# Performance work log

Hardware: AMD Instinct MI355X
Metric: run time of the kernel (lower is better)

Reference implementation:

```python
import jax, jax.numpy as jnp
import numpy as np

TEMPERATURE = 0.05
SCALE = 0.02  # keeps distances/T small enough that exp(-d/T) does not underflow


def setup_inputs() -> dict:
    key = jax.random.key(0)
    k1, k2 = jax.random.split(key)
    B, D = 4096, 1024
    text_embeddings = jax.random.normal(k1, (B, D), dtype=jnp.float32) * SCALE
    image_embeddings = jax.random.normal(k2, (B, D), dtype=jnp.float32) * SCALE
    return {"text_embeddings": text_embeddings, "image_embeddings": image_embeddings}


def reference(text_embeddings, image_embeddings):
    B = text_embeddings.shape[0]
    # Pairwise L2 distances between every image_i and every text_j without
    # materializing a [B, B, D] diff tensor: ||a||^2 + ||b||^2 - 2 a.b
    img_sq = jnp.sum(image_embeddings * image_embeddings, axis=1)   # [B]
    txt_sq = jnp.sum(text_embeddings * text_embeddings, axis=1)     # [B]
    cross = jnp.einsum('id,jd->ij', image_embeddings, text_embeddings)  # [B, B]
    sq_dist = img_sq[:, None] + txt_sq[None, :] - 2.0 * cross
    dist = jnp.sqrt(jnp.maximum(sq_dist, 0.0))                      # [B, B]
    sim = jnp.exp(-dist / TEMPERATURE)                              # [B, B]
    numerator = jnp.diagonal(sim)                                   # sim[i, i]
    denominator = jnp.sum(sim, axis=1) - numerator                  # off-diagonal row sum
    per_sample = jnp.where(denominator != 0.0,
                           -jnp.log(numerator / denominator),
                           0.0)
    return jnp.sum(per_sample) / B
```

## Files before the change

kernel.cpp:

```cpp
#include <hip/hip_runtime.h>
#include <hip/hip_bf16.h>
#include <math.h>

#define BSZ 4096
#define DSZ 1024
#define BM  256
#define BN  256
#define BK  64
#define NT  (DSZ / BK)

typedef unsigned short u16;
typedef __attribute__((ext_vector_type(8))) short bf16x8;
typedef __attribute__((ext_vector_type(4))) float f32x4;

__device__ inline u16 f2bf_rne(float f) {
    unsigned int u = __float_as_uint(f);
    u += 0x7fffu + ((u >> 16) & 1u);
    return (u16)(u >> 16);
}

__global__ __launch_bounds__(256) void cvt_norm_kernel(
        const float* __restrict__ img, const float* __restrict__ txt,
        u16* __restrict__ imgb, u16* __restrict__ txtb,
        float* __restrict__ img_sq, float* __restrict__ txt_sq,
        float* __restrict__ rowsum) {
    const int row = blockIdx.x;
    const bool isTxt = (blockIdx.y != 0);
    const float* __restrict__ src = isTxt ? txt : img;
    u16* __restrict__ dst = isTxt ? txtb : imgb;
    float* __restrict__ sq = isTxt ? txt_sq : img_sq;

    const int t = threadIdx.x;
    const float4 v = reinterpret_cast<const float4*>(src + (size_t)row * DSZ)[t];

    ushort4 o;
    o.x = f2bf_rne(v.x); o.y = f2bf_rne(v.y);
    o.z = f2bf_rne(v.z); o.w = f2bf_rne(v.w);
    reinterpret_cast<ushort4*>(dst + (size_t)row * DSZ)[t] = o;

    float s = v.x * v.x + v.y * v.y + v.z * v.z + v.w * v.w;
    #pragma unroll
    for (int off = 32; off; off >>= 1) s += __shfl_down(s, off);

    __shared__ float lds[4];
    if ((t & 63) == 0) lds[t >> 6] = s;
    __syncthreads();
    if (t == 0) {
        sq[row] = lds[0] + lds[1] + lds[2] + lds[3];
        if (!isTxt) rowsum[row] = 0.0f;
    }
}

__global__ __launch_bounds__(512, 2) void fused_mfma_kernel(
        const u16* __restrict__ imgb, const u16* __restrict__ txtb,
        const float* __restrict__ img_sq, const float* __restrict__ txt_sq,
        float* __restrict__ rowsum, float* __restrict__ diag_dist) {

    extern __shared__ char smem[];

    const int bi = blockIdx.y;
    const int bj = blockIdx.x;
    const int tid  = threadIdx.x;
    const int lane = tid & 63;
    const int w    = tid >> 6;
    const int wr   = w >> 2;
    const int wc   = w & 3;
    const int lr   = lane >> 4;
    const int lc   = lane & 15;
    const int swz  = lc & 7;

    const int ib0 = bi * BM;
    const int jb0 = bj * BN;

    const int srow = tid >> 3;
    const int sch  = tid & 7;

    f32x4 acc[8][4] = {};

    auto stage8k = [&](const u16* __restrict__ src, int xoff, int b, int h,
                       int j, int rowbase, int kt) {
        const int row_h = j * 64 + srow;
        const int gch   = sch ^ (row_h & 7);
        const u16* g = src + (size_t)(rowbase + h * 128 + row_h) * DSZ
                           + kt * BK + gch * 8;
        char* dst = smem + xoff + b * 32768 + h * 16384 + j * 8192 + w * 1024;
        __builtin_amdgcn_global_load_lds(
            (const __attribute__((address_space(1))) void*)g,
            (__attribute__((address_space(3))) void*)dst, 16, 0, 0);
    };
    auto stageA = [&](int b, int kt) {
        stage8k(imgb, 0, b, 0, 0, ib0, kt);
        stage8k(imgb, 0, b, 0, 1, ib0, kt);
        stage8k(imgb, 0, b, 1, 0, ib0, kt);
        stage8k(imgb, 0, b, 1, 1, ib0, kt);
    };
    auto stageB = [&](int b, int kt) {
        stage8k(txtb, 65536, b, 0, 0, jb0, kt);
        stage8k(txtb, 65536, b, 0, 1, jb0, kt);
        stage8k(txtb, 65536, b, 1, 0, jb0, kt);
        stage8k(txtb, 65536, b, 1, 1, jb0, kt);
    };

    const char* Abase = smem + wr * 16384;
    const char* Bbase = smem + 65536 + (wc >> 1) * 16384;
    const int rboff = (wc & 1) * 64;

    stageA(0, 0);
    stageB(0, 0);
    __syncthreads();

    int cur = 0;
    for (int kt = 0; kt < NT; ++kt) {
        const int nxt = cur ^ 1;
        bf16x8 bfr[2][4];

        #pragma unroll
        for (int p = 0; p < 4; ++p) {
            bf16x8 afr[2][2];
            if (p == 0) {
                #pragma unroll
                for (int kk = 0; kk < 2; ++kk)
                    #pragma unroll
                    for (int n = 0; n < 4; ++n) {
                        const int rb = rboff + n * 16 + lc;
                        bfr[kk][n] = *reinterpret_cast<const bf16x8*>(
                            Bbase + cur * 32768 + rb * 128
                                  + (((kk * 4 + lr) ^ swz) * 16));
                    }
            }
            #pragma unroll
            for (int dm = 0; dm < 2; ++dm)
                #pragma unroll
                for (int kk = 0; kk < 2; ++kk) {
                    const int ra = (p * 2 + dm) * 16 + lc;
                    afr[dm][kk] = *reinterpret_cast<const bf16x8*>(
                        Abase + cur * 32768 + ra * 128
                              + (((kk * 4 + lr) ^ swz) * 16));
                }

            if (kt + 1 < NT) {
                if (p == 0) stageA(nxt, kt + 1);
                else if (p == 1) stageB(nxt, kt + 1);
            }

            __builtin_amdgcn_s_barrier();
            __builtin_amdgcn_s_setprio(1);
            #pragma unroll
            for (int dm = 0; dm < 2; ++dm)
                #pragma unroll
                for (int n = 0; n < 4; ++n)
                    #pragma unroll
                    for (int kk = 0; kk < 2; ++kk)
                        acc[p * 2 + dm][n] = __builtin_amdgcn_mfma_f32_16x16x32_bf16(
                            afr[dm][kk], bfr[kk][n], acc[p * 2 + dm][n], 0, 0, 0);
            __builtin_amdgcn_s_setprio(0);
            if (p < 3) __builtin_amdgcn_s_barrier();
        }
        __syncthreads();
        cur = nxt;
    }

    const int jw = jb0 + wc * 64;
    const int iw = ib0 + wr * 128;

    float tq[4];
    #pragma unroll
    for (int n = 0; n < 4; ++n) tq[n] = txt_sq[jw + n * 16 + lc];

    float rs[8][4];
    #pragma unroll
    for (int m = 0; m < 8; ++m) {
        #pragma unroll
        for (int j = 0; j < 4; ++j) {
            const int gi = iw + m * 16 + lr * 4 + j;
            const float iq = img_sq[gi];
            float s = 0.0f;
            #pragma unroll
            for (int n = 0; n < 4; ++n) {
                const float d2 = iq + tq[n] - 2.0f * acc[m][n][j];
                const float d  = sqrtf(fmaxf(d2, 0.0f));
                const float sim = __expf(-20.0f * d);
                s += sim;
                if (gi == jw + n * 16 + lc) diag_dist[gi] = d;
            }
            rs[m][j] = s;
        }
    }

    #pragma unroll
    for (int off = 1; off < 16; off <<= 1)
        #pragma unroll
        for (int m = 0; m < 8; ++m)
            #pragma unroll
            for (int j = 0; j < 4; ++j)
                rs[m][j] += __shfl_xor(rs[m][j], off);

    if (lc == 0) {
        #pragma unroll
        for (int m = 0; m < 8; ++m)
            #pragma unroll
            for (int j = 0; j < 4; ++j)
                atomicAdd(&rowsum[iw + m * 16 + lr * 4 + j], rs[m][j]);
    }
}

__global__ __launch_bounds__(256) void finalize_kernel(
        const float* __restrict__ rowsum, const float* __restrict__ diag_dist,
        float* __restrict__ out) {
    const int tid = threadIdx.x;
    float s = 0.0f;
    for (int i = tid; i < BSZ; i += 256) {
        const float d   = diag_dist[i];
        const float num = __expf(-20.0f * d);
        const float den = rowsum[i] - num;
        s += (den != 0.0f) ? (20.0f * d + logf(den)) : 0.0f;
    }
    #pragma unroll
    for (int off = 32; off; off >>= 1) s += __shfl_down(s, off);

    __shared__ float lds[4];
    if ((tid & 63) == 0) lds[tid >> 6] = s;
    __syncthreads();
    if (tid == 0) out[0] = (lds[0] + lds[1] + lds[2] + lds[3]) * (1.0f / (float)BSZ);
}

extern "C" void kernel_launch(void* const* d_in, const int* in_sizes, int n_in,
                              void* d_out, int out_size, void* d_ws, size_t ws_size,
                              hipStream_t stream) {
    const float* txt = (const float*)d_in[0];
    const float* img = (const float*)d_in[1];
    float* out = (float*)d_out;

    u16* imgb = (u16*)d_ws;
    u16* txtb = imgb + (size_t)BSZ * DSZ;
    float* fws     = (float*)(txtb + (size_t)BSZ * DSZ);
    float* rowsum  = fws;
    float* diag    = fws + BSZ;
    float* img_sq  = fws + 2 * BSZ;
    float* txt_sq  = fws + 3 * BSZ;

    (void)hipFuncSetAttribute((const void*)fused_mfma_kernel,
                              hipFuncAttributeMaxDynamicSharedMemorySize, 131072);

    cvt_norm_kernel<<<dim3(BSZ, 2), 256, 0, stream>>>(img, txt, imgb, txtb,
                                                      img_sq, txt_sq, rowsum);

    fused_mfma_kernel<<<dim3(BSZ / BN, BSZ / BM), 512, 131072, stream>>>(
        imgb, txtb, img_sq, txt_sq, rowsum, diag);

    finalize_kernel<<<1, 256, 0, stream>>>(rowsum, diag, out);
}
```

Measured before the change: 129.0 us.

## Restructure GEMM mainloop into finer-grained staggered prefetch with explicit vmcnt waits

The k-loop now processes two k-tiles per iteration in eight phases. Each phase issues a half-tile global-to-LDS load, so the A and B prefetches for future tiles are spread across the loop and run further ahead. The full __syncthreads per tile is replaced by explicit s_waitcnt vmcnt/lgkmcnt plus s_barrier, so loads can stay in flight across phase boundaries. Block indices are also remapped to a swizzled order to improve L2 reuse between concurrently running tiles. The hand-counted vmcnt values are fragile: a wrong count could cause reads of LDS data that has not arrived yet.

```diff
diff --git a/kernel.cpp b/kernel.cpp
--- a/kernel.cpp
+++ b/kernel.cpp
@@ -7,7 +7,8 @@
 #define BM  256
 #define BN  256
 #define BK  64
-#define NT  (DSZ / BK)
+#define NT  16
+#define NIT 8
 
 typedef unsigned short u16;
 typedef __attribute__((ext_vector_type(8))) short bf16x8;
@@ -58,8 +59,10 @@
 
     extern __shared__ char smem[];
 
-    const int bi = blockIdx.y;
-    const int bj = blockIdx.x;
+    const int lin = blockIdx.y * 16 + blockIdx.x;
+    const int sw  = (lin & 7) * 32 + (lin >> 3);
+    const int bi = sw >> 4, bj = sw & 15;
+
     const int tid  = threadIdx.x;
     const int lane = tid & 63;
     const int w    = tid >> 6;
@@ -72,78 +75,77 @@
     const int ib0 = bi * BM;
     const int jb0 = bj * BN;
 
-    const int srow = tid >> 3;
-    const int sch  = tid & 7;
+    auto stageHT = [&](int mat, int kt, int h) {
+        const u16* base   = mat ? txtb : imgb;
+        const int rowbase = mat ? jb0 : ib0;
+        const int xoff    = mat ? 65536 : 0;
+        const int b = kt & 1;
+        #pragma unroll
+        for (int j = 0; j < 2; ++j) {
+            const int row_h = j * 64 + (tid >> 3);
+            const int gch   = (tid & 7) ^ (row_h & 7);
+            const u16* g = base + (size_t)(rowbase + h * 128 + row_h) * DSZ
+                                + kt * BK + gch * 8;
+            char* dst = smem + xoff + b * 32768 + h * 16384 + j * 8192 + w * 1024;
+            __builtin_amdgcn_global_load_lds(
+                (const __attribute__((address_space(1))) void*)g,
+                (__attribute__((address_space(3))) void*)dst, 16, 0, 0);
+        }
+    };
+
+    stageHT(0, 0, 0); stageHT(0, 0, 1);
+    stageHT(1, 0, 0); stageHT(1, 0, 1);
+    stageHT(1, 1, 0); stageHT(1, 1, 1);
+    asm volatile("s_waitcnt vmcnt(4)" ::: "memory");
+    __builtin_amdgcn_s_barrier();
 
     f32x4 acc[8][4] = {};
-
-    auto stage8k = [&](const u16* __restrict__ src, int xoff, int b, int h,
-                       int j, int rowbase, int kt) {
-        const int row_h = j * 64 + srow;
-        const int gch   = sch ^ (row_h & 7);
-        const u16* g = src + (size_t)(rowbase + h * 128 + row_h) * DSZ
-                           + kt * BK + gch * 8;
-        char* dst = smem + xoff + b * 32768 + h * 16384 + j * 8192 + w * 1024;
-        __builtin_amdgcn_global_load_lds(
-            (const __attribute__((address_space(1))) void*)g,
-            (__attribute__((address_space(3))) void*)dst, 16, 0, 0);
-    };
-    auto stageA = [&](int b, int kt) {
-        stage8k(imgb, 0, b, 0, 0, ib0, kt);
-        stage8k(imgb, 0, b, 0, 1, ib0, kt);
-        stage8k(imgb, 0, b, 1, 0, ib0, kt);
-        stage8k(imgb, 0, b, 1, 1, ib0, kt);
-    };
-    auto stageB = [&](int b, int kt) {
-        stage8k(txtb, 65536, b, 0, 0, jb0, kt);
-        stage8k(txtb, 65536, b, 0, 1, jb0, kt);
-        stage8k(txtb, 65536, b, 1, 0, jb0, kt);
-        stage8k(txtb, 65536, b, 1, 1, jb0, kt);
-    };
-
-    const char* Abase = smem + wr * 16384;
-    const char* Bbase = smem + 65536 + (wc >> 1) * 16384;
+    bf16x8 bfr[2][4];
+
+    const char* Ab[2] = { smem + wr * 16384,
+                          smem + 32768 + wr * 16384 };
+    const char* Bb[2] = { smem + 65536 + (wc >> 1) * 16384,
+                          smem + 65536 + 32768 + (wc >> 1) * 16384 };
     const int rboff = (wc & 1) * 64;
 
-    stageA(0, 0);
-    stageB(0, 0);
-    __syncthreads();
-
-    int cur = 0;
-    for (int kt = 0; kt < NT; ++kt) {
-        const int nxt = cur ^ 1;
-        bf16x8 bfr[2][4];
-
-        #pragma unroll
-        for (int p = 0; p < 4; ++p) {
-            bf16x8 afr[2][2];
-            if (p == 0) {
+    for (int i = 0; i < NIT; ++i) {
+        const bool more = (i < NIT - 1);
+        #pragma unroll
+        for (int p = 0; p < 8; ++p) {
+            const int tsel = p >> 2;
+            const int q    = p & 3;
+
+            if (q == 0) {
                 #pragma unroll
                 for (int kk = 0; kk < 2; ++kk)
                     #pragma unroll
-                    for (int n = 0; n < 4; ++n) {
-                        const int rb = rboff + n * 16 + lc;
+                    for (int n = 0; n < 4; ++n)
                         bfr[kk][n] = *reinterpret_cast<const bf16x8*>(
-                            Bbase + cur * 32768 + rb * 128
-                                  + (((kk * 4 + lr) ^ swz) * 16));
-                    }
+                            Bb[tsel] + (rboff + n * 16 + lc) * 128
+                                     + (((kk * 4 + lr) ^ swz) * 16));
             }
+            bf16x8 afr[2][2];
             #pragma unroll
             for (int dm = 0; dm < 2; ++dm)
                 #pragma unroll
-                for (int kk = 0; kk < 2; ++kk) {
-                    const int ra = (p * 2 + dm) * 16 + lc;
+                for (int kk = 0; kk < 2; ++kk)
                     afr[dm][kk] = *reinterpret_cast<const bf16x8*>(
-                        Abase + cur * 32768 + ra * 128
-                              + (((kk * 4 + lr) ^ swz) * 16));
-                }
-
-            if (kt + 1 < NT) {
-                if (p == 0) stageA(nxt, kt + 1);
-                else if (p == 1) stageB(nxt, kt + 1);
-            }
+                        Ab[tsel] + ((q * 2 + dm) * 16 + lc) * 128
+                                 + (((kk * 4 + lr) ^ swz) * 16));
+
+            if (p == 0)      stageHT(0, 2 * i + 1, 0);
+            else if (p == 1) stageHT(0, 2 * i + 1, 1);
+            else if (p == 2) { if (more) stageHT(1, 2 * i + 2, 0); }
+            else if (p == 3) { if (more) stageHT(1, 2 * i + 2, 1); }
+            else if (p == 4) { if (more) stageHT(0, 2 * i + 2, 0); }
+            else if (p == 5) { if (more) stageHT(0, 2 * i + 2, 1); }
+            else if (p == 6) { if (more) stageHT(1, 2 * i + 3, 0); }
+            else             { if (more) stageHT(1, 2 * i + 3, 1); }
 
             __builtin_amdgcn_s_barrier();
+            asm volatile("s_waitcnt lgkmcnt(0)" ::: "memory");
+            __builtin_amdgcn_sched_barrier(0);
+
             __builtin_amdgcn_s_setprio(1);
             #pragma unroll
             for (int dm = 0; dm < 2; ++dm)
@@ -151,13 +153,18 @@
                 for (int n = 0; n < 4; ++n)
                     #pragma unroll
                     for (int kk = 0; kk < 2; ++kk)
-                        acc[p * 2 + dm][n] = __builtin_amdgcn_mfma_f32_16x16x32_bf16(
-                            afr[dm][kk], bfr[kk][n], acc[p * 2 + dm][n], 0, 0, 0);
+                        acc[q * 2 + dm][n] = __builtin_amdgcn_mfma_f32_16x16x32_bf16(
+                            afr[dm][kk], bfr[kk][n], acc[q * 2 + dm][n], 0, 0, 0);
             __builtin_amdgcn_s_setprio(0);
-            if (p < 3) __builtin_amdgcn_s_barrier();
+
+            if (p == 3) {
+                if (more) asm volatile("s_waitcnt vmcnt(4)" ::: "memory");
+                else      asm volatile("s_waitcnt vmcnt(0)" ::: "memory");
+            } else if (p == 7) {
+                if (more) asm volatile("s_waitcnt vmcnt(4)" ::: "memory");
+            }
+            __builtin_amdgcn_s_barrier();
         }
-        __syncthreads();
-        cur = nxt;
     }
 
     const int jw = jb0 + wc * 64;
```

After: 127.8 us. About the same (-0.9%).
